# Kernel tuning notes

Hardware: AMD Instinct MI355X
Metric: run time of the kernel (lower is better)

Reference implementation:

```python
import jax, jax.numpy as jnp
import numpy as np

DIM = 1024
HEADS = 16
SEQ = 1024
N_EXP = 2
SLOTS = SEQ // N_EXP  # slots per expert; total slots == seq_len as in SoftMoE(dim, seq_len, num_experts)
HID = 4 * DIM         # expert FFN hidden
EPS = 1e-5


def layernorm(x, g, b):
    mu = x.mean(-1, keepdims=True)
    var = x.var(-1, keepdims=True)
    return (x - mu) * jax.lax.rsqrt(var + EPS) * g + b


def setup_inputs() -> dict:
    key = jax.random.key(0)
    ks = jax.random.split(key, 16)
    s = lambda k, shape, scale=0.02: jax.random.normal(k, shape, jnp.float32) * scale
    return {
        "x": jax.random.normal(ks[0], (4, SEQ, DIM), jnp.float32),
        "Wq": s(ks[1], (DIM, DIM)), "bq": jnp.zeros((DIM,), jnp.float32),
        "Wkv": s(ks[2], (DIM, 2 * DIM)), "bkv": jnp.zeros((2 * DIM,), jnp.float32),
        "Wp": s(ks[3], (DIM, DIM)), "bp": jnp.zeros((DIM,), jnp.float32),
        "g1": jnp.ones((DIM,), jnp.float32), "b1": jnp.zeros((DIM,), jnp.float32),
        "phi": s(ks[4], (DIM, N_EXP, SLOTS)),
        "We1": s(ks[5], (N_EXP, DIM, HID)), "be1": jnp.zeros((N_EXP, HID), jnp.float32),
        "We2": s(ks[6], (N_EXP, HID, DIM)), "be2": jnp.zeros((N_EXP, DIM), jnp.float32),
        "g2": jnp.ones((DIM,), jnp.float32), "b2": jnp.zeros((DIM,), jnp.float32),
    }


def soft_moe(x, phi, We1, be1, We2, be2):
    # x: [b,n,d]; phi: [d,e,s]
    logits = jnp.einsum("bnd,des->bnes", x, phi)
    dispatch = jax.nn.softmax(logits, axis=1)                    # over sequence
    b, n, e, s = logits.shape
    combine = jax.nn.softmax(logits.reshape(b, n, e * s), axis=-1).reshape(b, n, e, s)
    slots = jnp.einsum("bnd,bnes->besd", x, dispatch)            # [b,e,s,d]
    h = jax.nn.gelu(jnp.einsum("besd,edh->besh", slots, We1) + be1[None, :, None, :])
    y = jnp.einsum("besh,ehd->besd", h, We2) + be2[None, :, None, :]
    return jnp.einsum("besd,bnes->bnd", y, combine)


def reference(x, Wq, bq, Wkv, bkv, Wp, bp, g1, b1, phi, We1, be1, We2, be2, g2, b2):
    b, n, c = x.shape
    hd = c // HEADS
    scale = hd ** -0.5
    q = (x @ Wq + bq).reshape(b, n, HEADS, hd)
    kv = (x @ Wkv + bkv).reshape(b, n, 2, HEADS, hd)
    k, v = kv[:, :, 0], kv[:, :, 1]
    attn = jnp.einsum("bnhd,bmhd->bnmh", q, k) * scale
    attn = jax.nn.softmax(attn, axis=2)
    out = jnp.einsum("bnmh,bmhd->bnhd", attn, v).reshape(b, n, c)
    out = out @ Wp + bp
    x1 = layernorm(out + x, g1, b1)
    x2 = x1 + soft_moe(x1, phi, We1, be1, We2, be2)
    y = layernorm(x2 + x1, g2, b2)
    return (y, attn)
```

## Files before the change

kernel.cpp:

```cpp
#include <hip/hip_runtime.h>
#include <math.h>

#define BATCH 4
#define SEQ   1024
#define DIM   1024
#define HEADS 16
#define HD    64
#define NEXP  2
#define NSLOT 512
#define ES    1024
#define HID   4096
#define LNEPS 1e-5f
#define NTOK  (BATCH*SEQ)

typedef long long ll;
typedef unsigned short ushort;
typedef unsigned int uint;
typedef __attribute__((ext_vector_type(8))) short short8;
typedef __attribute__((ext_vector_type(4))) float f32x4;
typedef __attribute__((ext_vector_type(4))) unsigned short us4;

__device__ __forceinline__ ushort f2b(float f) {
    uint u = __builtin_bit_cast(uint, f);
    u += 0x7FFFu + ((u >> 16) & 1u);
    return (ushort)(u >> 16);
}
__device__ __forceinline__ float b2f(ushort h) {
    uint u = ((uint)h) << 16;
    return __builtin_bit_cast(float, u);
}
__device__ __forceinline__ uint pk(float a, float b) {
    return (uint)f2b(a) | ((uint)f2b(b) << 16);
}
__device__ __forceinline__ float gelu_f(float v) {
    float x3 = v * v * v;
    return 0.5f * v * (1.f + tanhf(0.7978845608028654f * (v + 0.044715f * x3)));
}

__device__ __forceinline__ void gload16(const ushort* g, ushort* l) {
    __builtin_amdgcn_global_load_lds(
        (const __attribute__((address_space(1))) unsigned int*)(const void*)g,
        (__attribute__((address_space(3))) unsigned int*)(void*)l,
        16, 0, 0);
}

__global__ __launch_bounds__(256) void cvt_bf16(
    const float* __restrict__ src, ushort* __restrict__ dst)
{
    int i = blockIdx.x * 256 + threadIdx.x;
    const float4* s = reinterpret_cast<const float4*>(src) + (ll)i * 2;
    float4 a = s[0], b = s[1];
    uint4 w;
    w.x = pk(a.x, a.y); w.y = pk(a.z, a.w);
    w.z = pk(b.x, b.y); w.w = pk(b.z, b.w);
    reinterpret_cast<uint4*>(dst)[i] = w;
}

template<typename TS>
__global__ __launch_bounds__(256) void transpose_cvt(
    const TS* __restrict__ src, int ldsrc, ll sS1, ll sS2,
    ushort* __restrict__ dst, int lddst, ll sD1, ll sD2, int Z2)
{
    __shared__ ushort tile[64][68];
    const int z1 = blockIdx.z / Z2, z2 = blockIdx.z % Z2;
    src += z1 * sS1 + z2 * sS2;
    dst += z1 * sD1 + z2 * sD2;
    const int r0 = blockIdx.y * 64, c0 = blockIdx.x * 64;
    const int t = threadIdx.x;
    #pragma unroll
    for (int j = 0; j < 4; j++) {
        int idx = t + 256 * j;
        int r = idx >> 4, c = (idx & 15) * 4;
        if constexpr (sizeof(TS) == 4) {
            float4 v = *reinterpret_cast<const float4*>(src + (ll)(r0 + r) * ldsrc + c0 + c);
            tile[r][c]     = f2b(v.x);
            tile[r][c + 1] = f2b(v.y);
            tile[r][c + 2] = f2b(v.z);
            tile[r][c + 3] = f2b(v.w);
        } else {
            *reinterpret_cast<us4*>(&tile[r][c]) =
                *reinterpret_cast<const us4*>(src + (ll)(r0 + r) * ldsrc + c0 + c);
        }
    }
    __syncthreads();
    #pragma unroll
    for (int j = 0; j < 4; j++) {
        int idx = t + 256 * j;
        int rr = idx >> 4, cc = (idx & 15) * 4;
        us4 w;
        w.x = tile[cc][rr]; w.y = tile[cc + 1][rr];
        w.z = tile[cc + 2][rr]; w.w = tile[cc + 3][rr];
        *reinterpret_cast<us4*>(&dst[(ll)(c0 + rr) * lddst + r0 + cc]) = w;
    }
}

template<int WR, int WC, int MI, int NI, int ACT, typename TC>
__global__ __launch_bounds__(256) void gemm_bf16(
    const ushort* __restrict__ A, int lda, ll sA1, ll sA2,
    const ushort* __restrict__ B, int ldb, ll sB1, ll sB2,
    const float* __restrict__ bias, ll sb1, ll sb2,
    TC* __restrict__ C, int ldc, ll sC1, ll sC2,
    int K, int Z2, float alpha)
{
    constexpr int BM = WR * MI * 16;
    constexpr int BN = WC * NI * 16;
    __shared__ alignas(16) ushort As[BM * 32];
    __shared__ alignas(16) ushort Bs[BN * 32];

    const int z1 = blockIdx.z / Z2, z2 = blockIdx.z % Z2;
    A += z1 * sA1 + z2 * sA2;
    B += z1 * sB1 + z2 * sB2;
    C += z1 * sC1 + z2 * sC2;

    const int t = threadIdx.x;
    const int m0 = blockIdx.y * BM, n0 = blockIdx.x * BN;
    const int lane = t & 63, wave = t >> 6;
    const int quad = lane >> 4, l16 = lane & 15;
    const int wm = wave / WC, wn = wave % WC;

    f32x4 acc[MI][NI] = {};

    for (int k0 = 0; k0 < K; k0 += 32) {
        #pragma unroll
        for (int i = 0; i < BM / 64; i++) {
            int seg = i * 256 + t;
            int row = seg >> 2, ke = (seg & 3) * 8;
            gload16(A + (ll)(m0 + row) * lda + (k0 + ke), &As[seg * 8]);
        }
        #pragma unroll
        for (int i = 0; i < BN / 64; i++) {
            int seg = i * 256 + t;
            int row = seg >> 2, ke = (seg & 3) * 8;
            gload16(B + (ll)(n0 + row) * ldb + (k0 + ke), &Bs[seg * 8]);
        }
        __syncthreads();

        short8 a[MI], b[NI];
        #pragma unroll
        for (int mi = 0; mi < MI; mi++)
            a[mi] = *reinterpret_cast<const short8*>(
                &As[(wm * MI * 16 + mi * 16 + l16) * 32 + quad * 8]);
        #pragma unroll
        for (int ni = 0; ni < NI; ni++)
            b[ni] = *reinterpret_cast<const short8*>(
                &Bs[(wn * NI * 16 + ni * 16 + l16) * 32 + quad * 8]);
        #pragma unroll
        for (int mi = 0; mi < MI; mi++)
            #pragma unroll
            for (int ni = 0; ni < NI; ni++)
                acc[mi][ni] = __builtin_amdgcn_mfma_f32_16x16x32_bf16(
                    a[mi], b[ni], acc[mi][ni], 0, 0, 0);
        __syncthreads();
    }

    const float* bz = bias ? (bias + z1 * sb1 + z2 * sb2) : nullptr;
    #pragma unroll
    for (int mi = 0; mi < MI; mi++) {
        #pragma unroll
        for (int ni = 0; ni < NI; ni++) {
            const int row = m0 + wm * MI * 16 + mi * 16 + quad * 4;
            const int col = n0 + wn * NI * 16 + ni * 16 + l16;
            const float bv = bz ? bz[col] : 0.f;
            #pragma unroll
            for (int r = 0; r < 4; r++) {
                float v = alpha * acc[mi][ni][r] + bv;
                if (ACT) v = gelu_f(v);
                if constexpr (sizeof(TC) == 2)
                    C[(ll)(row + r) * ldc + col] = f2b(v);
                else
                    C[(ll)(row + r) * ldc + col] = v;
            }
        }
    }
}

__global__ __launch_bounds__(256) void attn_softmax(
    ushort* __restrict__ p, float* __restrict__ attn_out)
{
    __shared__ float tile[16 * 1024];
    const int n = blockIdx.x, b = blockIdx.y;
    const int lane = threadIdx.x & 63, w = threadIdx.x >> 6;
    for (int hq = 0; hq < 4; hq++) {
        int h = hq * 4 + w;
        ushort* row = p + ((ll)(b * HEADS + h) * SEQ + n) * SEQ;
        float v[16];
        float m = -3.0e38f;
        #pragma unroll
        for (int j = 0; j < 16; j++) { v[j] = b2f(row[lane + 64 * j]); m = fmaxf(m, v[j]); }
        #pragma unroll
        for (int o = 32; o; o >>= 1) m = fmaxf(m, __shfl_xor(m, o));
        float s = 0.f;
        #pragma unroll
        for (int j = 0; j < 16; j++) { v[j] = __expf(v[j] - m); s += v[j]; }
        #pragma unroll
        for (int o = 32; o; o >>= 1) s += __shfl_xor(s, o);
        float inv = 1.f / s;
        int sw = (h & 7) << 2;
        #pragma unroll
        for (int j = 0; j < 16; j++) {
            float e = v[j] * inv;
            int mm = lane + 64 * j;
            row[mm] = f2b(e);
            tile[h * 1024 + (mm ^ sw)] = e;
        }
    }
    __syncthreads();
    float* outp = attn_out + ((ll)b * SEQ + n) * SEQ * HEADS;
    for (int o = threadIdx.x; o < SEQ * HEADS; o += 256) {
        int mm = o >> 4, h = o & 15;
        outp[o] = tile[h * 1024 + (mm ^ ((h & 7) << 2))];
    }
}

__global__ __launch_bounds__(256) void ln_kernel(
    const float* __restrict__ a, const float* __restrict__ b, float coef,
    const float* __restrict__ g, const float* __restrict__ beta,
    float* __restrict__ out, ushort* __restrict__ out_bf)
{
    const int row = blockIdx.x;
    const float* ar = a + (ll)row * DIM;
    const float* br = b + (ll)row * DIM;
    float v[4];
    float s1 = 0.f, s2 = 0.f;
    #pragma unroll
    for (int j = 0; j < 4; j++) {
        int i = threadIdx.x + 256 * j;
        v[j] = ar[i] + coef * br[i];
        s1 += v[j]; s2 += v[j] * v[j];
    }
    __shared__ float red[8];
    #pragma unroll
    for (int o = 32; o; o >>= 1) { s1 += __shfl_xor(s1, o); s2 += __shfl_xor(s2, o); }
    int w = threadIdx.x >> 6;
    if ((threadIdx.x & 63) == 0) { red[w] = s1; red[4 + w] = s2; }
    __syncthreads();
    s1 = red[0] + red[1] + red[2] + red[3];
    s2 = red[4] + red[5] + red[6] + red[7];
    float mu = s1 * (1.f / DIM);
    float var = s2 * (1.f / DIM) - mu * mu;
    float rs = rsqrtf(var + LNEPS);
    float* orow = out + (ll)row * DIM;
    #pragma unroll
    for (int j = 0; j < 4; j++) {
        int i = threadIdx.x + 256 * j;
        float val = (v[j] - mu) * rs * g[i] + beta[i];
        orow[i] = val;
        if (out_bf) out_bf[(ll)row * DIM + i] = f2b(val);
    }
}

__global__ __launch_bounds__(256) void col_softmax(
    const float* __restrict__ logits, ushort* __restrict__ dispT)
{
    const int b = blockIdx.x, cc = blockIdx.y;
    const int cl = threadIdx.x & 63;
    const int c = cc * 64 + cl;
    const int rg = threadIdx.x >> 6;
    const float* L = logits + (ll)b * SEQ * ES + c;
    ushort* DT = dispT + (ll)b * ES * SEQ + (ll)c * SEQ;
    __shared__ float red[4][64];
    float m = -3.0e38f;
    for (int n = rg; n < SEQ; n += 4) m = fmaxf(m, L[(ll)n * ES]);
    red[rg][cl] = m;
    __syncthreads();
    m = fmaxf(fmaxf(red[0][cl], red[1][cl]), fmaxf(red[2][cl], red[3][cl]));
    __syncthreads();
    float s = 0.f;
    for (int n = rg; n < SEQ; n += 4) s += __expf(L[(ll)n * ES] - m);
    red[rg][cl] = s;
    __syncthreads();
    s = red[0][cl] + red[1][cl] + red[2][cl] + red[3][cl];
    float inv = 1.f / s;
    for (int n = rg; n < SEQ; n += 4)
        DT[n] = f2b(__expf(L[(ll)n * ES] - m) * inv);
}

__global__ __launch_bounds__(256) void row_softmax(
    const float* __restrict__ logits, ushort* __restrict__ comb)
{
    const int row = blockIdx.x;
    const float* L = logits + (ll)row * ES;
    ushort* O = comb + (ll)row * ES;
    float v[4];
    float m = -3.0e38f;
    #pragma unroll
    for (int j = 0; j < 4; j++) { v[j] = L[threadIdx.x + 256 * j]; m = fmaxf(m, v[j]); }
    __shared__ float red[8];
    #pragma unroll
    for (int o = 32; o; o >>= 1) m = fmaxf(m, __shfl_xor(m, o));
    int w = threadIdx.x >> 6;
    if ((threadIdx.x & 63) == 0) red[w] = m;
    __syncthreads();
    m = fmaxf(fmaxf(red[0], red[1]), fmaxf(red[2], red[3]));
    __syncthreads();
    float s = 0.f;
    #pragma unroll
    for (int j = 0; j < 4; j++) { v[j] = __expf(v[j] - m); s += v[j]; }
    #pragma unroll
    for (int o = 32; o; o >>= 1) s += __shfl_xor(s, o);
    if ((threadIdx.x & 63) == 0) red[4 + w] = s;
    __syncthreads();
    s = red[4] + red[5] + red[6] + red[7];
    float inv = 1.f / s;
    #pragma unroll
    for (int j = 0; j < 4; j++) O[threadIdx.x + 256 * j] = f2b(v[j] * inv);
}

extern "C" void kernel_launch(void* const* d_in, const int* in_sizes, int n_in,
                              void* d_out, int out_size, void* d_ws, size_t ws_size,
                              hipStream_t stream)
{
    const float* x   = (const float*)d_in[0];
    const float* Wq  = (const float*)d_in[1];
    const float* bq  = (const float*)d_in[2];
    const float* Wkv = (const float*)d_in[3];
    const float* bkv = (const float*)d_in[4];
    const float* Wp  = (const float*)d_in[5];
    const float* bp  = (const float*)d_in[6];
    const float* g1  = (const float*)d_in[7];
    const float* b1  = (const float*)d_in[8];
    const float* phi = (const float*)d_in[9];
    const float* We1 = (const float*)d_in[10];
    const float* be1 = (const float*)d_in[11];
    const float* We2 = (const float*)d_in[12];
    const float* be2 = (const float*)d_in[13];
    const float* g2  = (const float*)d_in[14];
    const float* b2  = (const float*)d_in[15];

    float* out_y    = (float*)d_out;
    float* out_attn = out_y + (ll)BATCH * SEQ * DIM;

    const ll M1 = 1024 * 1024;
    float*  ws    = (float*)d_ws;
    ushort* x_bf  = (ushort*)(ws);
    ushort* WqT   = (ushort*)(ws + 2 * M1);
    ushort* WkvT  = (ushort*)(ws + 5 * M1 / 2);
    ushort* WpT   = (ushort*)(ws + 7 * M1 / 2);
    ushort* phiT  = (ushort*)(ws + 4 * M1);
    ushort* kv_bf = (ushort*)(ws + 9 * M1 / 2);
    ushort* We1T  = (ushort*)(ws + 9 * M1 / 2);
    ushort* vT    = (ushort*)(ws + 17 * M1 / 2);
    ushort* We2T  = (ushort*)(ws + 17 * M1 / 2);
    ushort* q_bf  = (ushort*)(ws + 21 * M1 / 2);
    ushort* p_bf  = (ushort*)(ws + 25 * M1 / 2);
    float*  po    = ws + 25 * M1 / 2;
    ushort* ao_bf = (ushort*)(ws + 89 * M1 / 2);
    ushort* ymoeT = (ushort*)(ws + 89 * M1 / 2);
    float*  x1    = ws + 33 * M1 / 2;
    ushort* x1_bf = (ushort*)(ws + 41 * M1 / 2);
    ushort* x1T   = (ushort*)(ws + 45 * M1 / 2);
    float*  logit = ws + 49 * M1 / 2;
    ushort* dispT = (ushort*)(ws + 57 * M1 / 2);
    ushort* comb  = (ushort*)(ws + 61 * M1 / 2);
    ushort* slots = (ushort*)(ws + 65 * M1 / 2);
    ushort* hmid  = (ushort*)(ws + 69 * M1 / 2);
    ushort* ymoe  = (ushort*)(ws + 85 * M1 / 2);
    float*  moe   = ws;

    dim3 blk(256);

    cvt_bf16<<<dim3(2048), blk, 0, stream>>>(x, x_bf);
    transpose_cvt<float><<<dim3(16, 16, 1), blk, 0, stream>>>(
        Wq, DIM, 0, 0, WqT, DIM, 0, 0, 1);
    transpose_cvt<float><<<dim3(32, 16, 1), blk, 0, stream>>>(
        Wkv, 2 * DIM, 0, 0, WkvT, DIM, 0, 0, 1);
    transpose_cvt<float><<<dim3(16, 16, 1), blk, 0, stream>>>(
        Wp, DIM, 0, 0, WpT, DIM, 0, 0, 1);
    transpose_cvt<float><<<dim3(16, 16, 1), blk, 0, stream>>>(
        phi, ES, 0, 0, phiT, DIM, 0, 0, 1);

    gemm_bf16<2,2,4,4,0,ushort><<<dim3(8, 32, 1), blk, 0, stream>>>(
        x_bf, DIM, 0, 0, WqT, DIM, 0, 0, bq, 0, 0,
        q_bf, DIM, 0, 0, DIM, 1, 1.f);
    gemm_bf16<2,2,4,4,0,ushort><<<dim3(16, 32, 1), blk, 0, stream>>>(
        x_bf, DIM, 0, 0, WkvT, DIM, 0, 0, bkv, 0, 0,
        kv_bf, 2 * DIM, 0, 0, DIM, 1, 1.f);

    transpose_cvt<ushort><<<dim3(1, 16, BATCH * HEADS), blk, 0, stream>>>(
        kv_bf + DIM, 2 * DIM, (ll)SEQ * 2 * DIM, HD,
        vT, SEQ, (ll)HEADS * HD * SEQ, (ll)HD * SEQ, HEADS);

    gemm_bf16<2,2,4,4,0,ushort><<<dim3(8, 8, BATCH * HEADS), blk, 0, stream>>>(
        q_bf, DIM, (ll)SEQ * DIM, HD,
        kv_bf, 2 * DIM, (ll)SEQ * 2 * DIM, HD,
        nullptr, 0, 0,
        p_bf, SEQ, (ll)HEADS * SEQ * SEQ, (ll)SEQ * SEQ,
        HD, HEADS, 0.125f);

    attn_softmax<<<dim3(SEQ, BATCH), blk, 0, stream>>>(p_bf, out_attn);

    gemm_bf16<4,1,2,4,0,ushort><<<dim3(1, 8, BATCH * HEADS), blk, 0, stream>>>(
        p_bf, SEQ, (ll)HEADS * SEQ * SEQ, (ll)SEQ * SEQ,
        vT, SEQ, (ll)HEADS * HD * SEQ, (ll)HD * SEQ,
        nullptr, 0, 0,
        ao_bf, DIM, (ll)SEQ * DIM, HD,
        SEQ, HEADS, 1.f);

    gemm_bf16<2,2,4,4,0,float><<<dim3(8, 32, 1), blk, 0, stream>>>(
        ao_bf, DIM, 0, 0, WpT, DIM, 0, 0, bp, 0, 0,
        po, DIM, 0, 0, DIM, 1, 1.f);
    ln_kernel<<<dim3(NTOK), blk, 0, stream>>>(po, x, 1.0f, g1, b1, x1, x1_bf);

    transpose_cvt<float><<<dim3(64, 16, 2), blk, 0, stream>>>(
        We1, HID, 0, (ll)DIM * HID, We1T, DIM, 0, (ll)HID * DIM, 2);
    transpose_cvt<float><<<dim3(16, 64, 2), blk, 0, stream>>>(
        We2, DIM, 0, (ll)HID * DIM, We2T, HID, 0, (ll)DIM * HID, 2);
    transpose_cvt<ushort><<<dim3(16, 16, BATCH), blk, 0, stream>>>(
        x1_bf, DIM, (ll)SEQ * DIM, 0, x1T, SEQ, (ll)DIM * SEQ, 0, 1);

    gemm_bf16<2,2,4,4,0,float><<<dim3(8, 32, 1), blk, 0, stream>>>(
        x1_bf, DIM, 0, 0, phiT, DIM, 0, 0, nullptr, 0, 0,
        logit, ES, 0, 0, DIM, 1, 1.f);
    col_softmax<<<dim3(BATCH, 16), blk, 0, stream>>>(logit, dispT);
    row_softmax<<<dim3(NTOK), blk, 0, stream>>>(logit, comb);

    gemm_bf16<2,2,4,4,0,ushort><<<dim3(8, 8, BATCH), blk, 0, stream>>>(
        dispT, SEQ, (ll)ES * SEQ, 0,
        x1T, SEQ, (ll)DIM * SEQ, 0,
        nullptr, 0, 0,
        slots, DIM, (ll)ES * DIM, 0,
        SEQ, 1, 1.f);

    gemm_bf16<2,2,4,4,1,ushort><<<dim3(32, 4, BATCH * NEXP), blk, 0, stream>>>(
        slots, DIM, (ll)ES * DIM, (ll)NSLOT * DIM,
        We1T, DIM, 0, (ll)HID * DIM,
        be1, 0, HID,
        hmid, HID, (ll)ES * HID, (ll)NSLOT * HID,
        DIM, NEXP, 1.f);

    gemm_bf16<2,2,4,4,0,ushort><<<dim3(8, 4, BATCH * NEXP), blk, 0, stream>>>(
        hmid, HID, (ll)ES * HID, (ll)NSLOT * HID,
        We2T, HID, 0, (ll)DIM * HID,
        be2, 0, DIM,
        ymoe, DIM, (ll)ES * DIM, (ll)NSLOT * DIM,
        HID, NEXP, 1.f);

    transpose_cvt<ushort><<<dim3(16, 16, BATCH), blk, 0, stream>>>(
        ymoe, DIM, (ll)ES * DIM, 0, ymoeT, ES, (ll)DIM * ES, 0, 1);

    gemm_bf16<2,2,4,4,0,float><<<dim3(8, 8, BATCH), blk, 0, stream>>>(
        comb, ES, (ll)SEQ * ES, 0,
        ymoeT, ES, (ll)DIM * ES, 0,
        nullptr, 0, 0,
        moe, DIM, (ll)SEQ * DIM, 0,
        ES, 1, 1.f);

    ln_kernel<<<dim3(NTOK), blk, 0, stream>>>(moe, x1, 2.0f, g2, b2, out_y, nullptr);
}
```

Baseline: 1.060 ms.

## Fuse Q and KV projections into one GEMM and vectorize softmax and layernorm

Concatenates the transposed Wq and Wkv weights and their biases so the Q, K and V projections run as a single GEMM with a 3*DIM-wide output. Later kernels now index into the combined qkv buffer. The attention softmax now reads and writes each row with 16-byte vector accesses and writes the fp32 attention output in per-head-group chunks through a smaller LDS tile. The layernorm uses float4 loads and stores. The aim is to cut kernel launches, improve memory coalescing and reduce LDS use, at the cost of an extra bias-concat kernel and more barriers in the softmax.

```diff
diff --git a/kernel.cpp b/kernel.cpp
--- a/kernel.cpp
+++ b/kernel.cpp
@@ -54,6 +54,14 @@
     w.x = pk(a.x, a.y); w.y = pk(a.z, a.w);
     w.z = pk(b.x, b.y); w.w = pk(b.z, b.w);
     reinterpret_cast<uint4*>(dst)[i] = w;
+}
+
+__global__ __launch_bounds__(256) void concat_bias(
+    const float* __restrict__ a, const float* __restrict__ b,
+    float* __restrict__ o)
+{
+    int i = blockIdx.x * 256 + threadIdx.x;
+    o[i] = (i < DIM) ? a[i] : b[i - DIM];
 }
 
 template<typename TS>
@@ -177,16 +185,26 @@
 __global__ __launch_bounds__(256) void attn_softmax(
     ushort* __restrict__ p, float* __restrict__ attn_out)
 {
-    __shared__ float tile[16 * 1024];
+    __shared__ float tile[4][1024];
     const int n = blockIdx.x, b = blockIdx.y;
-    const int lane = threadIdx.x & 63, w = threadIdx.x >> 6;
-    for (int hq = 0; hq < 4; hq++) {
-        int h = hq * 4 + w;
-        ushort* row = p + ((ll)(b * HEADS + h) * SEQ + n) * SEQ;
+    const int t = threadIdx.x;
+    const int lane = t & 63, w = t >> 6;
+    float* outp = attn_out + ((ll)b * SEQ + n) * SEQ * HEADS;
+    #pragma unroll 1
+    for (int g = 0; g < 4; g++) {
+        const int h = g * 4 + w;
+        ushort* row = p + ((ll)(b * HEADS + h) * SEQ + n) * SEQ + lane * 16;
+        uint4 r0 = reinterpret_cast<const uint4*>(row)[0];
+        uint4 r1 = reinterpret_cast<const uint4*>(row)[1];
+        uint rr[8] = {r0.x, r0.y, r0.z, r0.w, r1.x, r1.y, r1.z, r1.w};
         float v[16];
         float m = -3.0e38f;
         #pragma unroll
-        for (int j = 0; j < 16; j++) { v[j] = b2f(row[lane + 64 * j]); m = fmaxf(m, v[j]); }
+        for (int j = 0; j < 8; j++) {
+            v[2 * j]     = b2f((ushort)(rr[j] & 0xFFFFu));
+            v[2 * j + 1] = b2f((ushort)(rr[j] >> 16));
+            m = fmaxf(m, fmaxf(v[2 * j], v[2 * j + 1]));
+        }
         #pragma unroll
         for (int o = 32; o; o >>= 1) m = fmaxf(m, __shfl_xor(m, o));
         float s = 0.f;
@@ -194,21 +212,39 @@
         for (int j = 0; j < 16; j++) { v[j] = __expf(v[j] - m); s += v[j]; }
         #pragma unroll
         for (int o = 32; o; o >>= 1) s += __shfl_xor(s, o);
-        float inv = 1.f / s;
-        int sw = (h & 7) << 2;
-        #pragma unroll
-        for (int j = 0; j < 16; j++) {
-            float e = v[j] * inv;
-            int mm = lane + 64 * j;
-            row[mm] = f2b(e);
-            tile[h * 1024 + (mm ^ sw)] = e;
-        }
-    }
-    __syncthreads();
-    float* outp = attn_out + ((ll)b * SEQ + n) * SEQ * HEADS;
-    for (int o = threadIdx.x; o < SEQ * HEADS; o += 256) {
-        int mm = o >> 4, h = o & 15;
-        outp[o] = tile[h * 1024 + (mm ^ ((h & 7) << 2))];
+        const float inv = 1.f / s;
+        #pragma unroll
+        for (int j = 0; j < 16; j++) v[j] *= inv;
+        uint pw[8];
+        #pragma unroll
+        for (int j = 0; j < 8; j++) pw[j] = pk(v[2 * j], v[2 * j + 1]);
+        uint4 w0, w1;
+        w0.x = pw[0]; w0.y = pw[1]; w0.z = pw[2]; w0.w = pw[3];
+        w1.x = pw[4]; w1.y = pw[5]; w1.z = pw[6]; w1.w = pw[7];
+        reinterpret_cast<uint4*>(row)[0] = w0;
+        reinterpret_cast<uint4*>(row)[1] = w1;
+        const int sw = (h & 7) << 2;
+        #pragma unroll
+        for (int jj = 0; jj < 4; jj++) {
+            float4 f4;
+            f4.x = v[4 * jj]; f4.y = v[4 * jj + 1];
+            f4.z = v[4 * jj + 2]; f4.w = v[4 * jj + 3];
+            *reinterpret_cast<float4*>(&tile[w][(lane * 16 + 4 * jj) ^ sw]) = f4;
+        }
+        __syncthreads();
+        const int c0 = ((4 * g + 0) & 7) << 2, c1 = ((4 * g + 1) & 7) << 2;
+        const int c2 = ((4 * g + 2) & 7) << 2, c3 = ((4 * g + 3) & 7) << 2;
+        #pragma unroll
+        for (int jj = 0; jj < 4; jj++) {
+            int mm = t + 256 * jj;
+            float4 o4;
+            o4.x = tile[0][mm ^ c0];
+            o4.y = tile[1][mm ^ c1];
+            o4.z = tile[2][mm ^ c2];
+            o4.w = tile[3][mm ^ c3];
+            *reinterpret_cast<float4*>(&outp[(ll)mm * HEADS + 4 * g]) = o4;
+        }
+        __syncthreads();
     }
 }
 
@@ -218,34 +254,37 @@
     float* __restrict__ out, ushort* __restrict__ out_bf)
 {
     const int row = blockIdx.x;
-    const float* ar = a + (ll)row * DIM;
-    const float* br = b + (ll)row * DIM;
-    float v[4];
-    float s1 = 0.f, s2 = 0.f;
-    #pragma unroll
-    for (int j = 0; j < 4; j++) {
-        int i = threadIdx.x + 256 * j;
-        v[j] = ar[i] + coef * br[i];
-        s1 += v[j]; s2 += v[j] * v[j];
-    }
+    const int t = threadIdx.x;
+    float4 av = reinterpret_cast<const float4*>(a + (ll)row * DIM)[t];
+    float4 bv = reinterpret_cast<const float4*>(b + (ll)row * DIM)[t];
+    float4 v;
+    v.x = av.x + coef * bv.x; v.y = av.y + coef * bv.y;
+    v.z = av.z + coef * bv.z; v.w = av.w + coef * bv.w;
+    float s1 = v.x + v.y + v.z + v.w;
+    float s2 = v.x * v.x + v.y * v.y + v.z * v.z + v.w * v.w;
     __shared__ float red[8];
     #pragma unroll
     for (int o = 32; o; o >>= 1) { s1 += __shfl_xor(s1, o); s2 += __shfl_xor(s2, o); }
-    int w = threadIdx.x >> 6;
-    if ((threadIdx.x & 63) == 0) { red[w] = s1; red[4 + w] = s2; }
+    int w = t >> 6;
+    if ((t & 63) == 0) { red[w] = s1; red[4 + w] = s2; }
     __syncthreads();
     s1 = red[0] + red[1] + red[2] + red[3];
     s2 = red[4] + red[5] + red[6] + red[7];
     float mu = s1 * (1.f / DIM);
     float var = s2 * (1.f / DIM) - mu * mu;
     float rs = rsqrtf(var + LNEPS);
-    float* orow = out + (ll)row * DIM;
-    #pragma unroll
-    for (int j = 0; j < 4; j++) {
-        int i = threadIdx.x + 256 * j;
-        float val = (v[j] - mu) * rs * g[i] + beta[i];
-        orow[i] = val;
-        if (out_bf) out_bf[(ll)row * DIM + i] = f2b(val);
+    float4 gv = reinterpret_cast<const float4*>(g)[t];
+    float4 be = reinterpret_cast<const float4*>(beta)[t];
+    float4 o;
+    o.x = (v.x - mu) * rs * gv.x + be.x;
+    o.y = (v.y - mu) * rs * gv.y + be.y;
+    o.z = (v.z - mu) * rs * gv.z + be.z;
+    o.w = (v.w - mu) * rs * gv.w + be.w;
+    reinterpret_cast<float4*>(out + (ll)row * DIM)[t] = o;
+    if (out_bf) {
+        us4 hv;
+        hv.x = f2b(o.x); hv.y = f2b(o.y); hv.z = f2b(o.z); hv.w = f2b(o.w);
+        reinterpret_cast<us4*>(out_bf + (ll)row * DIM)[t] = hv;
     }
 }
 
@@ -331,58 +370,55 @@
     float* out_attn = out_y + (ll)BATCH * SEQ * DIM;
 
     const ll M1 = 1024 * 1024;
-    float*  ws    = (float*)d_ws;
-    ushort* x_bf  = (ushort*)(ws);
-    ushort* WqT   = (ushort*)(ws + 2 * M1);
-    ushort* WkvT  = (ushort*)(ws + 5 * M1 / 2);
-    ushort* WpT   = (ushort*)(ws + 7 * M1 / 2);
-    ushort* phiT  = (ushort*)(ws + 4 * M1);
-    ushort* kv_bf = (ushort*)(ws + 9 * M1 / 2);
-    ushort* We1T  = (ushort*)(ws + 9 * M1 / 2);
-    ushort* vT    = (ushort*)(ws + 17 * M1 / 2);
-    ushort* We2T  = (ushort*)(ws + 17 * M1 / 2);
-    ushort* q_bf  = (ushort*)(ws + 21 * M1 / 2);
-    ushort* p_bf  = (ushort*)(ws + 25 * M1 / 2);
-    float*  po    = ws + 25 * M1 / 2;
-    ushort* ao_bf = (ushort*)(ws + 89 * M1 / 2);
-    ushort* ymoeT = (ushort*)(ws + 89 * M1 / 2);
-    float*  x1    = ws + 33 * M1 / 2;
-    ushort* x1_bf = (ushort*)(ws + 41 * M1 / 2);
-    ushort* x1T   = (ushort*)(ws + 45 * M1 / 2);
-    float*  logit = ws + 49 * M1 / 2;
-    ushort* dispT = (ushort*)(ws + 57 * M1 / 2);
-    ushort* comb  = (ushort*)(ws + 61 * M1 / 2);
-    ushort* slots = (ushort*)(ws + 65 * M1 / 2);
-    ushort* hmid  = (ushort*)(ws + 69 * M1 / 2);
-    ushort* ymoe  = (ushort*)(ws + 85 * M1 / 2);
-    float*  moe   = ws;
+    float*  ws     = (float*)d_ws;
+    ushort* x_bf   = (ushort*)(ws);
+    ushort* WqkvT  = (ushort*)(ws + 2 * M1);
+    ushort* WpT    = (ushort*)(ws + 7 * M1 / 2);
+    ushort* phiT   = (ushort*)(ws + 4 * M1);
+    ushort* qkv_bf = (ushort*)(ws + 9 * M1 / 2);
+    ushort* vT     = (ushort*)(ws + 21 * M1 / 2);
+    ushort* p_bf   = (ushort*)(ws + 25 * M1 / 2);
+    float*  po     = ws + 25 * M1 / 2;
+    ushort* ao_bf  = (ushort*)(ws + 89 * M1 / 2);
+    ushort* ymoeT  = (ushort*)(ws + 89 * M1 / 2);
+    float*  x1     = ws + 33 * M1 / 2;
+    ushort* x1_bf  = (ushort*)(ws + 41 * M1 / 2);
+    ushort* x1T    = (ushort*)(ws + 45 * M1 / 2);
+    float*  logit  = ws + 49 * M1 / 2;
+    ushort* dispT  = (ushort*)(ws + 57 * M1 / 2);
+    ushort* comb   = (ushort*)(ws + 61 * M1 / 2);
+    ushort* slots  = (ushort*)(ws + 65 * M1 / 2);
+    ushort* hmid   = (ushort*)(ws + 69 * M1 / 2);
+    ushort* ymoe   = (ushort*)(ws + 85 * M1 / 2);
+    ushort* We1T   = (ushort*)(ws + 9 * M1 / 2);
+    ushort* We2T   = (ushort*)(ws + 17 * M1 / 2);
+    float*  bqkv   = ws + 93 * M1 / 2;
+    float*  moe    = ws;
 
     dim3 blk(256);
 
     cvt_bf16<<<dim3(2048), blk, 0, stream>>>(x, x_bf);
     transpose_cvt<float><<<dim3(16, 16, 1), blk, 0, stream>>>(
-        Wq, DIM, 0, 0, WqT, DIM, 0, 0, 1);
+        Wq, DIM, 0, 0, WqkvT, DIM, 0, 0, 1);
     transpose_cvt<float><<<dim3(32, 16, 1), blk, 0, stream>>>(
-        Wkv, 2 * DIM, 0, 0, WkvT, DIM, 0, 0, 1);
+        Wkv, 2 * DIM, 0, 0, WqkvT + (ll)DIM * DIM, DIM, 0, 0, 1);
     transpose_cvt<float><<<dim3(16, 16, 1), blk, 0, stream>>>(
         Wp, DIM, 0, 0, WpT, DIM, 0, 0, 1);
     transpose_cvt<float><<<dim3(16, 16, 1), blk, 0, stream>>>(
         phi, ES, 0, 0, phiT, DIM, 0, 0, 1);
-
-    gemm_bf16<2,2,4,4,0,ushort><<<dim3(8, 32, 1), blk, 0, stream>>>(
-        x_bf, DIM, 0, 0, WqT, DIM, 0, 0, bq, 0, 0,
-        q_bf, DIM, 0, 0, DIM, 1, 1.f);
-    gemm_bf16<2,2,4,4,0,ushort><<<dim3(16, 32, 1), blk, 0, stream>>>(
-        x_bf, DIM, 0, 0, WkvT, DIM, 0, 0, bkv, 0, 0,
-        kv_bf, 2 * DIM, 0, 0, DIM, 1, 1.f);
+    concat_bias<<<dim3(12), blk, 0, stream>>>(bq, bkv, bqkv);
+
+    gemm_bf16<2,2,4,4,0,ushort><<<dim3(24, 32, 1), blk, 0, stream>>>(
+        x_bf, DIM, 0, 0, WqkvT, DIM, 0, 0, bqkv, 0, 0,
+        qkv_bf, 3 * DIM, 0, 0, DIM, 1, 1.f);
 
     transpose_cvt<ushort><<<dim3(1, 16, BATCH * HEADS), blk, 0, stream>>>(
-        kv_bf + DIM, 2 * DIM, (ll)SEQ * 2 * DIM, HD,
+        qkv_bf + 2 * DIM, 3 * DIM, (ll)SEQ * 3 * DIM, HD,
         vT, SEQ, (ll)HEADS * HD * SEQ, (ll)HD * SEQ, HEADS);
 
     gemm_bf16<2,2,4,4,0,ushort><<<dim3(8, 8, BATCH * HEADS), blk, 0, stream>>>(
-        q_bf, DIM, (ll)SEQ * DIM, HD,
-        kv_bf, 2 * DIM, (ll)SEQ * 2 * DIM, HD,
+        qkv_bf, 3 * DIM, (ll)SEQ * 3 * DIM, HD,
+        qkv_bf + DIM, 3 * DIM, (ll)SEQ * 3 * DIM, HD,
         nullptr, 0, 0,
         p_bf, SEQ, (ll)HEADS * SEQ * SEQ, (ll)SEQ * SEQ,
         HD, HEADS, 0.125f);
```

Measured after the change: 1.190 ms. 1.12x slower.
